# Performance work log

Hardware: AMD Instinct MI355X
Metric: run time of the kernel (lower is better)

Reference implementation:

```python
import jax, jax.numpy as jnp
import numpy as np

INPUT, HIDDEN, C, H, W, PK = 64, 128, 16, 32, 32, 4
B, T = 512, 1024

def hardsigmoid(v):
    return jnp.clip(v / 6.0 + 0.5, 0.0, 1.0)

def setup_inputs() -> dict:
    key = jax.random.key(0)
    ks = jax.random.split(key, 9)
    s_rnn = 1.0 / np.sqrt(HIDDEN)
    s_map = 1.0 / np.sqrt(HIDDEN)
    return {
        "x": jax.random.normal(ks[0], (B, T, INPUT), dtype=jnp.float32),
        "W_ih": jax.random.uniform(ks[1], (HIDDEN, INPUT), minval=-s_rnn, maxval=s_rnn),
        "b_ih": jax.random.uniform(ks[2], (HIDDEN,), minval=-s_rnn, maxval=s_rnn),
        "W_hh": jax.random.uniform(ks[3], (HIDDEN, HIDDEN), minval=-s_rnn, maxval=s_rnn),
        "b_hh": jax.random.uniform(ks[4], (HIDDEN,), minval=-s_rnn, maxval=s_rnn),
        "W_gate": jax.random.uniform(ks[5], (HIDDEN, HIDDEN), minval=-s_rnn, maxval=s_rnn),
        "b_gate": jax.random.uniform(ks[6], (HIDDEN,), minval=-s_rnn, maxval=s_rnn),
        "W_map": jax.random.uniform(ks[7], (C * H * W, HIDDEN), minval=-s_map, maxval=s_map),
        "b_map": jax.random.uniform(ks[8], (C * H * W,), minval=-s_map, maxval=s_map),
    }

def reference(x, W_ih, b_ih, W_hh, b_hh, W_gate, b_gate, W_map, b_map):
    batch, seq_len, _ = x.shape
    h0 = jnp.zeros((batch, HIDDEN), dtype=x.dtype)
    agg0 = jnp.zeros((batch, HIDDEN), dtype=x.dtype)

    def step(carry, xt):
        h, agg = carry
        h = jnp.tanh(xt @ W_ih.T + b_ih + h @ W_hh.T + b_hh)
        gate = hardsigmoid(h @ W_gate.T + b_gate)
        return (h, agg + h * gate), None

    (h, agg), _ = jax.lax.scan(step, (h0, agg0), jnp.swapaxes(x, 0, 1))
    agg = agg / float(seq_len)

    mapped = (agg @ W_map.T + b_map).reshape(batch, C, H, W)
    # AvgPool2d(kernel=PK, stride=PK) via reshape-mean
    pooled = mapped.reshape(batch, C, H // PK, PK, W // PK, PK).mean(axis=(3, 5))
    upsampled = jnp.repeat(jnp.repeat(pooled, PK, axis=2), PK, axis=3)
    return mapped * hardsigmoid(upsampled)
```

## Files before the change

### kernel.cpp

```cpp
#include <hip/hip_runtime.h>
#include <hip/hip_bf16.h>

#define T_SEQ 1024
#define BATCH 512
#define INPUT 64
#define HID   128

typedef __attribute__((ext_vector_type(8))) short bf16x8;
typedef __attribute__((ext_vector_type(4))) short s16x4;
typedef __attribute__((ext_vector_type(4))) float f32x4;
typedef __attribute__((ext_vector_type(2))) unsigned int u32x2;

#define MFMA __builtin_amdgcn_mfma_f32_16x16x32_bf16

__device__ __forceinline__ short f2bf(float f) {
    union { float f; unsigned u; } v; v.f = f;
    unsigned r = (v.u + 0x7FFFu + ((v.u >> 16) & 1u)) >> 16;
    return (short)r;
}

__device__ __forceinline__ unsigned cvtpk_bf16(float lo, float hi) {
    unsigned r;
    asm("v_cvt_pk_bf16_f32 %0, %1, %2" : "=v"(r) : "v"(lo), "v"(hi));
    return r;
}

__device__ __forceinline__ float fast_tanh(float s) {
    float e = __expf(2.0f * s);
    return 1.0f - 2.0f * __builtin_amdgcn_rcpf(e + 1.0f);
}

__device__ __forceinline__ float hsig(float v) {
    return __builtin_amdgcn_fmed3f(v * 0.16666666666666666f + 0.5f, 0.0f, 1.0f);
}

__device__ __forceinline__ void wg_barrier_lds() {
    asm volatile("s_waitcnt lgkmcnt(0)" ::: "memory");
    __builtin_amdgcn_s_barrier();
    asm volatile("" ::: "memory");
}

__global__ __launch_bounds__(256) void cvt_kernel(const float* __restrict__ in,
                                                  short* __restrict__ out, int n4) {
    int i = blockIdx.x * 256 + threadIdx.x;
    if (i >= n4) return;
    f32x4 v = ((const f32x4*)in)[i];
    s16x4 o;
    #pragma unroll
    for (int j = 0; j < 4; ++j) o[j] = f2bf(v[j]);
    ((s16x4*)out)[i] = o;
}

__global__ __launch_bounds__(512, 1) void rnn_kernel(
    const float* __restrict__ xf_,
    const float* __restrict__ W_ih, const float* __restrict__ b_ih,
    const float* __restrict__ W_hh, const float* __restrict__ b_hh,
    const float* __restrict__ W_gate, const float* __restrict__ b_gate,
    float* __restrict__ agg_out)
{
    __shared__ __align__(16) short sh[2][16][136];

    const int tid  = threadIdx.x;
    const int wave = tid >> 6, lane = tid & 63;
    const int q = lane >> 4, l15 = lane & 15;
    const int b0 = blockIdx.x * 16;
    const int group = wave >> 2;
    const int gw = wave & 3;
    const int R0 = 32 * gw, R1 = R0 + 16;

    bf16x8 wih[2][2], whh[2][4], wgf[2][4];
    #pragma unroll
    for (int tile = 0; tile < 2; ++tile) {
        const int row = (tile ? R1 : R0) + l15;
        #pragma unroll
        for (int f = 0; f < 2; ++f) {
            const float* p = W_ih + row * INPUT + f * 32 + q * 8;
            bf16x8 v;
            #pragma unroll
            for (int j = 0; j < 8; ++j) v[j] = f2bf(p[j]);
            wih[tile][f] = v;
        }
        #pragma unroll
        for (int f = 0; f < 4; ++f) {
            const float* p = W_hh + row * HID + f * 32 + q * 8;
            bf16x8 v;
            #pragma unroll
            for (int j = 0; j < 8; ++j) v[j] = f2bf(p[j]);
            whh[tile][f] = v;
        }
        #pragma unroll
        for (int f = 0; f < 4; ++f) {
            const float* p = W_gate + row * HID + f * 32 + q * 8;
            bf16x8 v;
            #pragma unroll
            for (int j = 0; j < 8; ++j) v[j] = f2bf(p[j]);
            wgf[tile][f] = v;
        }
    }

    f32x4 bias1[2], biasg[2], zero4;
    #pragma unroll
    for (int tile = 0; tile < 2; ++tile) {
        const int rbase = (tile ? R1 : R0) + q * 4;
        #pragma unroll
        for (int r = 0; r < 4; ++r) {
            bias1[tile][r] = b_ih[rbase + r] + b_hh[rbase + r];
            biasg[tile][r] = b_gate[rbase + r];
        }
    }
    #pragma unroll
    for (int r = 0; r < 4; ++r) zero4[r] = 0.0f;

    f32x4 agg0 = zero4, agg1 = zero4;
    f32x4 hpA = zero4, hpB = zero4;
    f32x4 accx0, accx1;
    f32x4 P0, P1, P2, P3, Q0, Q1, Q2, Q3;

    const float* xf_lane = xf_ + ((long)(b0 + l15) * T_SEQ) * INPUT + q * 8;

    auto critical = [&](int t) {
        const int rb = (t & 1) ^ 1, wb = t & 1;
        bf16x8 hf0 = *(const bf16x8*)&sh[rb][l15][q * 8];
        bf16x8 hf1 = *(const bf16x8*)&sh[rb][l15][32 + q * 8];
        bf16x8 hf2 = *(const bf16x8*)&sh[rb][l15][64 + q * 8];
        bf16x8 hf3 = *(const bf16x8*)&sh[rb][l15][96 + q * 8];
        f32x4 a0 = MFMA(whh[0][0], hf0, accx0, 0, 0, 0);
        f32x4 c0 = MFMA(whh[0][2], hf2, zero4, 0, 0, 0);
        f32x4 a1 = MFMA(whh[1][0], hf0, accx1, 0, 0, 0);
        f32x4 c1 = MFMA(whh[1][2], hf2, zero4, 0, 0, 0);
        a0 = MFMA(whh[0][1], hf1, a0, 0, 0, 0);
        c0 = MFMA(whh[0][3], hf3, c0, 0, 0, 0);
        a1 = MFMA(whh[1][1], hf1, a1, 0, 0, 0);
        c1 = MFMA(whh[1][3], hf3, c1, 0, 0, 0);
        hpA[0] = fast_tanh(a0[0] + c0[0]);
        hpA[1] = fast_tanh(a0[1] + c0[1]);
        hpA[2] = fast_tanh(a0[2] + c0[2]);
        hpA[3] = fast_tanh(a0[3] + c0[3]);
        hpB[0] = fast_tanh(a1[0] + c1[0]);
        hpB[1] = fast_tanh(a1[1] + c1[1]);
        hpB[2] = fast_tanh(a1[2] + c1[2]);
        hpB[3] = fast_tanh(a1[3] + c1[3]);
        u32x2 p0, p1;
        p0[0] = cvtpk_bf16(hpA[0], hpA[1]); p0[1] = cvtpk_bf16(hpA[2], hpA[3]);
        p1[0] = cvtpk_bf16(hpB[0], hpB[1]); p1[1] = cvtpk_bf16(hpB[2], hpB[3]);
        *(u32x2*)&sh[wb][l15][R0 + q * 4] = p0;
        *(u32x2*)&sh[wb][l15][R1 + q * 4] = p1;
    };

    auto shadow = [&](int t, f32x4& r0, f32x4& r1, f32x4& r2, f32x4& r3) {
        const int rb = (t & 1) ^ 1;
        bf16x8 gf0 = *(const bf16x8*)&sh[rb][l15][q * 8];
        bf16x8 gf1 = *(const bf16x8*)&sh[rb][l15][32 + q * 8];
        bf16x8 gf2 = *(const bf16x8*)&sh[rb][l15][64 + q * 8];
        bf16x8 gf3 = *(const bf16x8*)&sh[rb][l15][96 + q * 8];
        bf16x8 fa, fb;
        #pragma unroll
        for (int j = 0; j < 4; ++j) {
            fa[j] = f2bf(r0[j]); fa[4 + j] = f2bf(r1[j]);
            fb[j] = f2bf(r2[j]); fb[4 + j] = f2bf(r3[j]);
        }
        accx0 = MFMA(wih[0][0], fa, bias1[0], 0, 0, 0);
        accx1 = MFMA(wih[1][0], fa, bias1[1], 0, 0, 0);
        accx0 = MFMA(wih[0][1], fb, accx0, 0, 0, 0);
        accx1 = MFMA(wih[1][1], fb, accx1, 0, 0, 0);
        int tt = t + 5; if (tt > T_SEQ - 1) tt = T_SEQ - 1;
        {
            const float* p = xf_lane + (long)tt * INPUT;
            r0 = *(const f32x4*)p;        r1 = *(const f32x4*)(p + 4);
            r2 = *(const f32x4*)(p + 32); r3 = *(const f32x4*)(p + 36);
        }
        f32x4 g0 = MFMA(wgf[0][0], gf0, biasg[0], 0, 0, 0);
        f32x4 e0 = MFMA(wgf[0][2], gf2, zero4, 0, 0, 0);
        f32x4 g1 = MFMA(wgf[1][0], gf0, biasg[1], 0, 0, 0);
        f32x4 e1 = MFMA(wgf[1][2], gf2, zero4, 0, 0, 0);
        g0 = MFMA(wgf[0][1], gf1, g0, 0, 0, 0);
        e0 = MFMA(wgf[0][3], gf3, e0, 0, 0, 0);
        g1 = MFMA(wgf[1][1], gf1, g1, 0, 0, 0);
        e1 = MFMA(wgf[1][3], gf3, e1, 0, 0, 0);
        #pragma unroll
        for (int r = 0; r < 4; ++r) {
            agg0[r] += hpA[r] * hsig(g0[r] + e0[r]);
            agg1[r] += hpB[r] * hsig(g1[r] + e1[r]);
        }
    };

    {
        const float* p = xf_lane + (long)group * INPUT;
        f32x4 a0 = *(const f32x4*)p,        a1 = *(const f32x4*)(p + 4);
        f32x4 a2 = *(const f32x4*)(p + 32), a3 = *(const f32x4*)(p + 36);
        bf16x8 ta, tb;
        #pragma unroll
        for (int j = 0; j < 4; ++j) {
            ta[j] = f2bf(a0[j]); ta[4 + j] = f2bf(a1[j]);
            tb[j] = f2bf(a2[j]); tb[4 + j] = f2bf(a3[j]);
        }
        accx0 = MFMA(wih[0][0], ta, bias1[0], 0, 0, 0);
        accx1 = MFMA(wih[1][0], ta, bias1[1], 0, 0, 0);
        accx0 = MFMA(wih[0][1], tb, accx0, 0, 0, 0);
        accx1 = MFMA(wih[1][1], tb, accx1, 0, 0, 0);
        if (group == 0) {
            hpA[0] = fast_tanh(accx0[0]); hpA[1] = fast_tanh(accx0[1]);
            hpA[2] = fast_tanh(accx0[2]); hpA[3] = fast_tanh(accx0[3]);
            hpB[0] = fast_tanh(accx1[0]); hpB[1] = fast_tanh(accx1[1]);
            hpB[2] = fast_tanh(accx1[2]); hpB[3] = fast_tanh(accx1[3]);
            u32x2 p0, p1;
            p0[0] = cvtpk_bf16(hpA[0], hpA[1]); p0[1] = cvtpk_bf16(hpA[2], hpA[3]);
            p1[0] = cvtpk_bf16(hpB[0], hpB[1]); p1[1] = cvtpk_bf16(hpB[2], hpB[3]);
            *(u32x2*)&sh[0][l15][R0 + q * 4] = p0;
            *(u32x2*)&sh[0][l15][R1 + q * 4] = p1;
        }
        const float* pp = xf_lane + (long)(group ? 3 : 2) * INPUT;
        P0 = *(const f32x4*)pp;        P1 = *(const f32x4*)(pp + 4);
        P2 = *(const f32x4*)(pp + 32); P3 = *(const f32x4*)(pp + 36);
        const float* pq = xf_lane + (long)(group ? 5 : 4) * INPUT;
        Q0 = *(const f32x4*)pq;        Q1 = *(const f32x4*)(pq + 4);
        Q2 = *(const f32x4*)(pq + 32); Q3 = *(const f32x4*)(pq + 36);
    }
    wg_barrier_lds();

    if (group == 0) {
        shadow(1, P0, P1, P2, P3);   wg_barrier_lds();
        critical(2);                 wg_barrier_lds();
        for (int i = 0; i < 255; ++i) {
            shadow(4 * i + 3, Q0, Q1, Q2, Q3); wg_barrier_lds();
            critical(4 * i + 4);               wg_barrier_lds();
            shadow(4 * i + 5, P0, P1, P2, P3); wg_barrier_lds();
            critical(4 * i + 6);               wg_barrier_lds();
        }
        shadow(1023, Q0, Q1, Q2, Q3); wg_barrier_lds();
    } else {
        critical(1);                 wg_barrier_lds();
        shadow(2, P0, P1, P2, P3);   wg_barrier_lds();
        for (int i = 0; i < 255; ++i) {
            critical(4 * i + 3);               wg_barrier_lds();
            shadow(4 * i + 4, Q0, Q1, Q2, Q3); wg_barrier_lds();
            critical(4 * i + 5);               wg_barrier_lds();
            shadow(4 * i + 6, P0, P1, P2, P3); wg_barrier_lds();
        }
        critical(1023); wg_barrier_lds();
    }

    if (group == 1) {
        bf16x8 gf0 = *(const bf16x8*)&sh[1][l15][q * 8];
        bf16x8 gf1 = *(const bf16x8*)&sh[1][l15][32 + q * 8];
        bf16x8 gf2 = *(const bf16x8*)&sh[1][l15][64 + q * 8];
        bf16x8 gf3 = *(const bf16x8*)&sh[1][l15][96 + q * 8];
        f32x4 g0 = MFMA(wgf[0][0], gf0, biasg[0], 0, 0, 0);
        f32x4 e0 = MFMA(wgf[0][2], gf2, zero4, 0, 0, 0);
        f32x4 g1 = MFMA(wgf[1][0], gf0, biasg[1], 0, 0, 0);
        f32x4 e1 = MFMA(wgf[1][2], gf2, zero4, 0, 0, 0);
        g0 = MFMA(wgf[0][1], gf1, g0, 0, 0, 0);
        e0 = MFMA(wgf[0][3], gf3, e0, 0, 0, 0);
        g1 = MFMA(wgf[1][1], gf1, g1, 0, 0, 0);
        e1 = MFMA(wgf[1][3], gf3, e1, 0, 0, 0);
        #pragma unroll
        for (int r = 0; r < 4; ++r) {
            agg0[r] += hpA[r] * hsig(g0[r] + e0[r]);
            agg1[r] += hpB[r] * hsig(g1[r] + e1[r]);
        }
    }
    wg_barrier_lds();

    float* aggf = (float*)&sh[0][0][0];
    if (group == 0) {
        *(f32x4*)&aggf[l15 * HID + R0 + q * 4] = agg0;
        *(f32x4*)&aggf[l15 * HID + R1 + q * 4] = agg1;
    }
    wg_barrier_lds();
    if (group == 1) {
        const float s = 1.0f / (float)T_SEQ;
        f32x4 t0 = *(const f32x4*)&aggf[l15 * HID + R0 + q * 4];
        f32x4 t1 = *(const f32x4*)&aggf[l15 * HID + R1 + q * 4];
        #pragma unroll
        for (int r = 0; r < 4; ++r) { t0[r] = (t0[r] + agg0[r]) * s; t1[r] = (t1[r] + agg1[r]) * s; }
        *(f32x4*)&agg_out[(long)(b0 + l15) * HID + R0 + q * 4] = t0;
        *(f32x4*)&agg_out[(long)(b0 + l15) * HID + R1 + q * 4] = t1;
    }
}

template<bool PRE>
__global__ __launch_bounds__(256) void map_kernel(
    const float* __restrict__ agg, const float* __restrict__ Wf,
    const short* __restrict__ Wb, const float* __restrict__ b_map,
    float* __restrict__ out)
{
    __shared__ float sh_pool[4][16][8];
    __shared__ float sh_gate[16][8];

    const int tid  = threadIdx.x;
    const int wave = tid >> 6, lane = tid & 63;
    const int q = lane >> 4, l15 = lane & 15;
    const int mb = blockIdx.x & 31;
    const int nb = blockIdx.x >> 5;
    const int b0 = mb * 16;
    const int n0 = nb * 128 + wave * 32;

    bf16x8 af[4];
    #pragma unroll
    for (int kb = 0; kb < 4; ++kb) {
        const float* p = agg + (b0 + l15) * HID + kb * 32 + q * 8;
        bf16x8 f;
        #pragma unroll
        for (int j = 0; j < 8; ++j) f[j] = f2bf(p[j]);
        af[kb] = f;
    }
    f32x4 cc[2];
    #pragma unroll
    for (int tn = 0; tn < 2; ++tn) {
        int nn = n0 + tn * 16 + l15;
        float bias = b_map[nn];
        f32x4 c;
        #pragma unroll
        for (int r = 0; r < 4; ++r) c[r] = bias;
        #pragma unroll
        for (int kb = 0; kb < 4; ++kb) {
            bf16x8 f;
            if (PRE) {
                f = *(const bf16x8*)(Wb + (long)nn * HID + kb * 32 + q * 8);
            } else {
                const float* p = Wf + (long)nn * HID + kb * 32 + q * 8;
                #pragma unroll
                for (int j = 0; j < 8; ++j) f[j] = f2bf(p[j]);
            }
            c = __builtin_amdgcn_mfma_f32_16x16x32_bf16(af[kb], f, c, 0, 0, 0);
        }
        cc[tn] = c;
        f32x4 t = c;
        #pragma unroll
        for (int r = 0; r < 4; ++r) {
            t[r] += __shfl_xor(t[r], 1);
            t[r] += __shfl_xor(t[r], 2);
        }
        if ((l15 & 3) == 0) {
            int pw = tn * 4 + (l15 >> 2);
            #pragma unroll
            for (int r = 0; r < 4; ++r) sh_pool[wave][q * 4 + r][pw] = t[r];
        }
    }
    __syncthreads();
    if (tid < 128) {
        int b = tid >> 3, pw = tid & 7;
        float s = sh_pool[0][b][pw] + sh_pool[1][b][pw] +
                  sh_pool[2][b][pw] + sh_pool[3][b][pw];
        sh_gate[b][pw] = hsig(s * (1.0f / 16.0f));
    }
    __syncthreads();
    #pragma unroll
    for (int tn = 0; tn < 2; ++tn) {
        int nn = n0 + tn * 16 + l15;
        int pw = tn * 4 + (l15 >> 2);
        #pragma unroll
        for (int r = 0; r < 4; ++r)
            out[(long)(b0 + q * 4 + r) * 16384 + nn] = cc[tn][r] * sh_gate[q * 4 + r][pw];
    }
}

extern "C" void kernel_launch(void* const* d_in, const int* in_sizes, int n_in,
                              void* d_out, int out_size, void* d_ws, size_t ws_size,
                              hipStream_t stream) {
    const float* x      = (const float*)d_in[0];
    const float* W_ih   = (const float*)d_in[1];
    const float* b_ih   = (const float*)d_in[2];
    const float* W_hh   = (const float*)d_in[3];
    const float* b_hh   = (const float*)d_in[4];
    const float* W_gate = (const float*)d_in[5];
    const float* b_gate = (const float*)d_in[6];
    const float* W_map  = (const float*)d_in[7];
    const float* b_map  = (const float*)d_in[8];
    float* out = (float*)d_out;

    const size_t wm_bytes = (size_t)16384 * HID * 2;
    const size_t agg_bytes = (size_t)BATCH * HID * 4;
    const bool pre = ws_size >= wm_bytes + agg_bytes;

    if (pre) {
        short* wm_bf = (short*)d_ws;
        float* agg   = (float*)((char*)d_ws + wm_bytes);

        cvt_kernel<<<(16384 * HID / 4 + 255) / 256, 256, 0, stream>>>(W_map, wm_bf, 16384 * HID / 4);
        rnn_kernel<<<32, 512, 0, stream>>>(x, W_ih, b_ih, W_hh, b_hh,
                                           W_gate, b_gate, agg);
        map_kernel<true><<<4096, 256, 0, stream>>>(agg, W_map, wm_bf, b_map, out);
    } else {
        float* agg = (float*)d_ws;
        rnn_kernel<<<32, 512, 0, stream>>>(x, W_ih, b_ih, W_hh, b_hh,
                                           W_gate, b_gate, agg);
        map_kernel<false><<<4096, 256, 0, stream>>>(agg, W_map, nullptr, b_map, out);
    }
}
```

Baseline: 769.2 us.

## Fold W_map bf16 conversion into extra RNN blocks and move x prefetch to critical phase

```diff
diff --git a/kernel.cpp b/kernel.cpp
--- a/kernel.cpp
+++ b/kernel.cpp
@@ -25,6 +25,15 @@
     return r;
 }
 
+__device__ __forceinline__ bf16x8 pack_bf16x8(f32x4 a, f32x4 b) {
+    union { unsigned u[4]; bf16x8 v; } r;
+    r.u[0] = cvtpk_bf16(a[0], a[1]);
+    r.u[1] = cvtpk_bf16(a[2], a[3]);
+    r.u[2] = cvtpk_bf16(b[0], b[1]);
+    r.u[3] = cvtpk_bf16(b[2], b[3]);
+    return r.v;
+}
+
 __device__ __forceinline__ float fast_tanh(float s) {
     float e = __expf(2.0f * s);
     return 1.0f - 2.0f * __builtin_amdgcn_rcpf(e + 1.0f);
@@ -40,24 +49,26 @@
     asm volatile("" ::: "memory");
 }
 
-__global__ __launch_bounds__(256) void cvt_kernel(const float* __restrict__ in,
-                                                  short* __restrict__ out, int n4) {
-    int i = blockIdx.x * 256 + threadIdx.x;
-    if (i >= n4) return;
-    f32x4 v = ((const f32x4*)in)[i];
-    s16x4 o;
-    #pragma unroll
-    for (int j = 0; j < 4; ++j) o[j] = f2bf(v[j]);
-    ((s16x4*)out)[i] = o;
-}
-
-__global__ __launch_bounds__(512, 1) void rnn_kernel(
+__global__ __launch_bounds__(512, 2) void rnn_kernel(
     const float* __restrict__ xf_,
     const float* __restrict__ W_ih, const float* __restrict__ b_ih,
     const float* __restrict__ W_hh, const float* __restrict__ b_hh,
     const float* __restrict__ W_gate, const float* __restrict__ b_gate,
-    float* __restrict__ agg_out)
+    float* __restrict__ agg_out,
+    const float* __restrict__ W_map, short* __restrict__ wm_bf)
 {
+    if (blockIdx.x >= 32) {
+        const int n4 = 16384 * HID / 4;
+        for (int i = (blockIdx.x - 32) * 512 + threadIdx.x; i < n4; i += 32 * 512) {
+            f32x4 v = ((const f32x4*)W_map)[i];
+            s16x4 o;
+            #pragma unroll
+            for (int j = 0; j < 4; ++j) o[j] = f2bf(v[j]);
+            ((s16x4*)wm_bf)[i] = o;
+        }
+        return;
+    }
+
     __shared__ __align__(16) short sh[2][16][136];
 
     const int tid  = threadIdx.x;
@@ -118,7 +129,14 @@
 
     const float* xf_lane = xf_ + ((long)(b0 + l15) * T_SEQ) * INPUT + q * 8;
 
-    auto critical = [&](int t) {
+    auto load_raw = [&](int tt, f32x4& r0, f32x4& r1, f32x4& r2, f32x4& r3) {
+        if (tt > T_SEQ - 1) tt = T_SEQ - 1;
+        const float* p = xf_lane + (long)tt * INPUT;
+        r0 = *(const f32x4*)p;        r1 = *(const f32x4*)(p + 4);
+        r2 = *(const f32x4*)(p + 32); r3 = *(const f32x4*)(p + 36);
+    };
+
+    auto critical = [&](int t, f32x4& r0, f32x4& r1, f32x4& r2, f32x4& r3) {
         const int rb = (t & 1) ^ 1, wb = t & 1;
         bf16x8 hf0 = *(const bf16x8*)&sh[rb][l15][q * 8];
         bf16x8 hf1 = *(const bf16x8*)&sh[rb][l15][32 + q * 8];
@@ -132,6 +150,7 @@
         c0 = MFMA(whh[0][3], hf3, c0, 0, 0, 0);
         a1 = MFMA(whh[1][1], hf1, a1, 0, 0, 0);
         c1 = MFMA(whh[1][3], hf3, c1, 0, 0, 0);
+        load_raw(t + 4, r0, r1, r2, r3);
         hpA[0] = fast_tanh(a0[0] + c0[0]);
         hpA[1] = fast_tanh(a0[1] + c0[1]);
         hpA[2] = fast_tanh(a0[2] + c0[2]);
@@ -153,22 +172,12 @@
         bf16x8 gf1 = *(const bf16x8*)&sh[rb][l15][32 + q * 8];
         bf16x8 gf2 = *(const bf16x8*)&sh[rb][l15][64 + q * 8];
         bf16x8 gf3 = *(const bf16x8*)&sh[rb][l15][96 + q * 8];
-        bf16x8 fa, fb;
-        #pragma unroll
-        for (int j = 0; j < 4; ++j) {
-            fa[j] = f2bf(r0[j]); fa[4 + j] = f2bf(r1[j]);
-            fb[j] = f2bf(r2[j]); fb[4 + j] = f2bf(r3[j]);
-        }
+        bf16x8 fa = pack_bf16x8(r0, r1);
+        bf16x8 fb = pack_bf16x8(r2, r3);
         accx0 = MFMA(wih[0][0], fa, bias1[0], 0, 0, 0);
         accx1 = MFMA(wih[1][0], fa, bias1[1], 0, 0, 0);
         accx0 = MFMA(wih[0][1], fb, accx0, 0, 0, 0);
         accx1 = MFMA(wih[1][1], fb, accx1, 0, 0, 0);
-        int tt = t + 5; if (tt > T_SEQ - 1) tt = T_SEQ - 1;
-        {
-            const float* p = xf_lane + (long)tt * INPUT;
-            r0 = *(const f32x4*)p;        r1 = *(const f32x4*)(p + 4);
-            r2 = *(const f32x4*)(p + 32); r3 = *(const f32x4*)(p + 36);
-        }
         f32x4 g0 = MFMA(wgf[0][0], gf0, biasg[0], 0, 0, 0);
         f32x4 e0 = MFMA(wgf[0][2], gf2, zero4, 0, 0, 0);
         f32x4 g1 = MFMA(wgf[1][0], gf0, biasg[1], 0, 0, 0);
@@ -185,15 +194,10 @@
     };
 
     {
-        const float* p = xf_lane + (long)group * INPUT;
-        f32x4 a0 = *(const f32x4*)p,        a1 = *(const f32x4*)(p + 4);
-        f32x4 a2 = *(const f32x4*)(p + 32), a3 = *(const f32x4*)(p + 36);
-        bf16x8 ta, tb;
-        #pragma unroll
-        for (int j = 0; j < 4; ++j) {
-            ta[j] = f2bf(a0[j]); ta[4 + j] = f2bf(a1[j]);
-            tb[j] = f2bf(a2[j]); tb[4 + j] = f2bf(a3[j]);
-        }
+        f32x4 a0, a1, a2, a3;
+        load_raw(group, a0, a1, a2, a3);
+        bf16x8 ta = pack_bf16x8(a0, a1);
+        bf16x8 tb = pack_bf16x8(a2, a3);
         accx0 = MFMA(wih[0][0], ta, bias1[0], 0, 0, 0);
         accx1 = MFMA(wih[1][0], ta, bias1[1], 0, 0, 0);
         accx0 = MFMA(wih[0][1], tb, accx0, 0, 0, 0);
@@ -208,36 +212,34 @@
             p1[0] = cvtpk_bf16(hpB[0], hpB[1]); p1[1] = cvtpk_bf16(hpB[2], hpB[3]);
             *(u32x2*)&sh[0][l15][R0 + q * 4] = p0;
             *(u32x2*)&sh[0][l15][R1 + q * 4] = p1;
-        }
-        const float* pp = xf_lane + (long)(group ? 3 : 2) * INPUT;
-        P0 = *(const f32x4*)pp;        P1 = *(const f32x4*)(pp + 4);
-        P2 = *(const f32x4*)(pp + 32); P3 = *(const f32x4*)(pp + 36);
-        const float* pq = xf_lane + (long)(group ? 5 : 4) * INPUT;
-        Q0 = *(const f32x4*)pq;        Q1 = *(const f32x4*)(pq + 4);
-        Q2 = *(const f32x4*)(pq + 32); Q3 = *(const f32x4*)(pq + 36);
+            load_raw(2, P0, P1, P2, P3);
+            load_raw(4, Q0, Q1, Q2, Q3);
+        } else {
+            load_raw(3, P0, P1, P2, P3);
+        }
     }
     wg_barrier_lds();
 
     if (group == 0) {
-        shadow(1, P0, P1, P2, P3);   wg_barrier_lds();
-        critical(2);                 wg_barrier_lds();
+        shadow(1, P0, P1, P2, P3);                 wg_barrier_lds();
+        critical(2, P0, P1, P2, P3);               wg_barrier_lds();
         for (int i = 0; i < 255; ++i) {
-            shadow(4 * i + 3, Q0, Q1, Q2, Q3); wg_barrier_lds();
-            critical(4 * i + 4);               wg_barrier_lds();
-            shadow(4 * i + 5, P0, P1, P2, P3); wg_barrier_lds();
-            critical(4 * i + 6);               wg_barrier_lds();
-        }
-        shadow(1023, Q0, Q1, Q2, Q3); wg_barrier_lds();
+            shadow(4 * i + 3, Q0, Q1, Q2, Q3);     wg_barrier_lds();
+            critical(4 * i + 4, Q0, Q1, Q2, Q3);   wg_barrier_lds();
+            shadow(4 * i + 5, P0, P1, P2, P3);     wg_barrier_lds();
+            critical(4 * i + 6, P0, P1, P2, P3);   wg_barrier_lds();
+        }
+        shadow(1023, Q0, Q1, Q2, Q3);              wg_barrier_lds();
     } else {
-        critical(1);                 wg_barrier_lds();
-        shadow(2, P0, P1, P2, P3);   wg_barrier_lds();
+        critical(1, Q0, Q1, Q2, Q3);               wg_barrier_lds();
+        shadow(2, P0, P1, P2, P3);                 wg_barrier_lds();
         for (int i = 0; i < 255; ++i) {
-            critical(4 * i + 3);               wg_barrier_lds();
-            shadow(4 * i + 4, Q0, Q1, Q2, Q3); wg_barrier_lds();
-            critical(4 * i + 5);               wg_barrier_lds();
-            shadow(4 * i + 6, P0, P1, P2, P3); wg_barrier_lds();
-        }
-        critical(1023); wg_barrier_lds();
+            critical(4 * i + 3, P0, P1, P2, P3);   wg_barrier_lds();
+            shadow(4 * i + 4, Q0, Q1, Q2, Q3);     wg_barrier_lds();
+            critical(4 * i + 5, Q0, Q1, Q2, Q3);   wg_barrier_lds();
+            shadow(4 * i + 6, P0, P1, P2, P3);     wg_barrier_lds();
+        }
+        critical(1023, P0, P1, P2, P3);            wg_barrier_lds();
     }
 
     if (group == 1) {
@@ -369,7 +371,7 @@
     const float* b_map  = (const float*)d_in[8];
     float* out = (float*)d_out;
 
-    const size_t wm_bytes = (size_t)16384 * HID * 2;
+    const size_t wm_bytes  = (size_t)16384 * HID * 2;
     const size_t agg_bytes = (size_t)BATCH * HID * 4;
     const bool pre = ws_size >= wm_bytes + agg_bytes;
 
@@ -377,14 +379,13 @@
         short* wm_bf = (short*)d_ws;
         float* agg   = (float*)((char*)d_ws + wm_bytes);
 
-        cvt_kernel<<<(16384 * HID / 4 + 255) / 256, 256, 0, stream>>>(W_map, wm_bf, 16384 * HID / 4);
-        rnn_kernel<<<32, 512, 0, stream>>>(x, W_ih, b_ih, W_hh, b_hh,
-                                           W_gate, b_gate, agg);
+        rnn_kernel<<<64, 512, 0, stream>>>(x, W_ih, b_ih, W_hh, b_hh,
+                                           W_gate, b_gate, agg, W_map, wm_bf);
         map_kernel<true><<<4096, 256, 0, stream>>>(agg, W_map, wm_bf, b_map, out);
     } else {
         float* agg = (float*)d_ws;
         rnn_kernel<<<32, 512, 0, stream>>>(x, W_ih, b_ih, W_hh, b_hh,
-                                           W_gate, b_gate, agg);
+                                           W_gate, b_gate, agg, nullptr, nullptr);
         map_kernel<false><<<4096, 256, 0, stream>>>(agg, W_map, nullptr, b_map, out);
     }
 }
```

New measurement: 880.8 us. +14.5%, slower.
